# Optimization experiments

Measured on AMD Instinct MI355X. Metric: run time of the kernel, lower is better.

The kernel has to match this reference:

```python
import jax, jax.numpy as jnp
import numpy as np

N, E, G = 10000, 100000, 16
NS, NV = 128, 64            # scalar (0e) / vector (1o) channel counts
DIM = NS + 3 * NV           # 320 flattened feature dim
NSP = 4                     # num_species; edge one-hot has NSP**2 entries
FC_IN = 128                 # edge length embedding size
GATES = NV                  # one gate scalar per gated vector channel
EPS = 1e-5


def _split(x):
    # flattened irreps layout: [NS scalars | NV vectors * 3 components]
    return x[:, :NS], x[:, NS:].reshape(x.shape[0], NV, 3)


def _merge(s, v):
    return jnp.concatenate([s, v.reshape(v.shape[0], -1)], axis=-1)


def setup_inputs() -> dict:
    key = jax.random.key(0)
    ks = jax.random.split(key, 32)
    def nrm(i, shape):
        return jax.random.normal(ks[i], shape, jnp.float32)
    return {
        'node_fea': nrm(0, (N, DIM)),
        'edge_one_hot': jax.random.uniform(ks[1], (E, NSP * NSP), jnp.float32),
        'edge_sh': nrm(2, (E, 4)),
        'edge_fea': nrm(3, (E, DIM)),
        'edge_length_embedded': jax.random.uniform(ks[4], (E, FC_IN), jnp.float32),
        'edge_index': jax.random.randint(ks[5], (2, E), 0, N),
        'batch': jnp.sort(jax.random.randint(ks[6], (N,), 0, G)),
        # self-connection FCTP: edge irreps x species-pair scalars -> out irreps
        'Wsc_s': nrm(7, (NS, NSP * NSP, NS)),
        'Wsc_v': nrm(8, (NV, NSP * NSP, NV)),
        # lin_pre (per-l equivariant linear, bias on scalars only)
        'Wpre0': nrm(9, (NS, NS)), 'bpre0': jnp.zeros((NS,), jnp.float32),
        'Wpre1': nrm(10, (NV, NV)),
        # separate-weight tensor product paths (fea_in x spherical harmonics)
        'Wss': nrm(11, (3 * NS, NS + GATES)),   # 0e x 0e -> 0e
        'Wvs': nrm(12, (3 * NV, NS + GATES)),   # 1o . 1o -> 0e
        'Wsv': nrm(13, (3 * NS, NV)),           # 0e x 1o -> 1o
        'Wvv': nrm(14, (3 * NV, NV)),           # 1o x 0e -> 1o
        # radial MLP (fc): edge_length_embedded -> per-channel conv weights
        'Wf1': nrm(15, (FC_IN, 64)) / np.sqrt(FC_IN), 'bf1': jnp.zeros((64,), jnp.float32),
        'Wf2': nrm(16, (64, 64)) / 8.0, 'bf2': jnp.zeros((64,), jnp.float32),
        'Wf3': nrm(17, (64, NS + NV)) / 8.0, 'bf3': jnp.zeros((NS + NV,), jnp.float32),
        # lin_post
        'Wpost0': nrm(18, (NS, NS)), 'bpost0': jnp.zeros((NS,), jnp.float32),
        'Wpost1': nrm(19, (NV, NV)),
        # e3LayerNorm affine params
        'gamma_s': jnp.ones((NS,), jnp.float32), 'beta_s': jnp.zeros((NS,), jnp.float32),
        'gamma_v': jnp.ones((NV,), jnp.float32),
    }


def reference(node_fea, edge_one_hot, edge_sh, edge_fea, edge_length_embedded,
              edge_index, batch, Wsc_s, Wsc_v, Wpre0, bpre0, Wpre1,
              Wss, Wvs, Wsv, Wvv, Wf1, bf1, Wf2, bf2, Wf3, bf3,
              Wpost0, bpost0, Wpost1, gamma_s, beta_s, gamma_v):
    i, j = edge_index[0], edge_index[1]
    batch_edge = batch[i]
    es, ev = _split(edge_fea)

    # --- self connection: FullyConnectedTensorProduct(edge_fea, one_hot) ---
    sc_s = jnp.einsum('ev,es,vsu->eu', es, edge_one_hot, Wsc_s) / np.sqrt(NS * NSP * NSP)
    sc_v = jnp.einsum('evm,es,vsu->eum', ev, edge_one_hot, Wsc_v) / np.sqrt(NV * NSP * NSP)

    # --- lin_pre on edge features ---
    s = es @ Wpre0 / np.sqrt(NS) + bpre0
    v = jnp.einsum('evm,vu->eum', ev, Wpre1) / np.sqrt(NV)

    # --- gather node features and concat along channel axis ---
    nsf, nvf = _split(node_fea)
    s_in = jnp.concatenate([nsf[i], nsf[j], s], axis=-1)   # [E, 3*NS]
    v_in = jnp.concatenate([nvf[i], nvf[j], v], axis=1)    # [E, 3*NV, 3]

    sh0, sh1 = edge_sh[:, :1], edge_sh[:, 1:4]
    # --- separate-weight tensor product (CG: 1o x 1o -> 0e via dot/sqrt(3)) ---
    out_s = (jnp.einsum('ev,vu->eu', s_in * sh0, Wss) / np.sqrt(3 * NS)
             + jnp.einsum('evm,em,vu->eu', v_in, sh1, Wvs) / np.sqrt(3 * 3 * NV)) / np.sqrt(2.0)
    out_v = (jnp.einsum('ev,em,vu->eum', s_in, sh1, Wsv) / np.sqrt(3 * NS)
             + jnp.einsum('evm,e,vu->eum', v_in, sh0[:, 0], Wvv) / np.sqrt(3 * NV)) / np.sqrt(2.0)

    # --- gate nonlinearity: silu on scalars, sigmoid gates on vectors ---
    z_s = jax.nn.silu(out_s[:, :NS])
    z_v = out_v * jax.nn.sigmoid(out_s[:, NS:])[:, :, None]

    # --- radial MLP -> e3ElementWise per-channel scaling ---
    h = jax.nn.silu(edge_length_embedded @ Wf1 + bf1)
    h = jax.nn.silu(h @ Wf2 + bf2)
    w = h @ Wf3 + bf3                                      # [E, NS+NV]
    z_s = z_s * w[:, :NS]
    z_v = z_v * w[:, NS:, None]

    # --- lin_post ---
    z_s = z_s @ Wpost0 / np.sqrt(NS) + bpost0
    z_v = jnp.einsum('evm,vu->eum', z_v, Wpost1) / np.sqrt(NV)

    # --- add self connection ---
    z_s = z_s + sc_s
    z_v = z_v + sc_v

    # --- e3LayerNorm with per-graph statistics over edges ---
    cnt = jax.ops.segment_sum(jnp.ones((E,), z_s.dtype), batch_edge, num_segments=G)
    cnt = jnp.maximum(cnt, 1.0)
    mean_s = jax.ops.segment_sum(z_s.sum(-1), batch_edge, num_segments=G) / (cnt * NS)
    z_s = z_s - mean_s[batch_edge][:, None]
    var_s = jax.ops.segment_sum((z_s ** 2).sum(-1), batch_edge, num_segments=G) / (cnt * NS)
    z_s = z_s * jax.lax.rsqrt(var_s + EPS)[batch_edge][:, None] * gamma_s + beta_s
    var_v = jax.ops.segment_sum((z_v ** 2).sum((-1, -2)), batch_edge, num_segments=G) / (cnt * NV * 3)
    z_v = z_v * jax.lax.rsqrt(var_v + EPS)[batch_edge][:, None, None] * gamma_v[None, :, None]

    # --- skip connection (same irreps in/out -> plain add) ---
    return edge_fea + _merge(z_s, z_v)
```

## Files before the change

### kernel.cpp

```cpp
#include <hip/hip_runtime.h>
#include <math.h>

typedef unsigned int u32;
typedef unsigned short u16;
typedef __attribute__((ext_vector_type(8))) short bf16x8;
typedef __attribute__((ext_vector_type(4))) float f32x4;

#define E_TOT 100000
constexpr int NS = 128, DIM = 320;

constexpr float SC_S_SCALE = 0.022097086912079608f;
constexpr float SC_V_SCALE = 0.03125f;
constexpr float INV_SQRT128 = 0.08838834764831845f;
constexpr float INV_8 = 0.125f;
constexpr float INV_S384 = 0.05103103630798288f;
constexpr float INV_24 = 0.041666666666666664f;
constexpr float INV_S192 = 0.07216878364870323f;
constexpr float RSQRT2 = 0.7071067811865476f;

#define MFMA __builtin_amdgcn_mfma_f32_16x16x32_bf16
#define F4Z (f32x4){0.f, 0.f, 0.f, 0.f}

__device__ __forceinline__ float sigmoidf_(float x) { return 1.0f / (1.0f + __expf(-x)); }
__device__ __forceinline__ float siluf_(float x) { return x * sigmoidf_(x); }
__device__ __forceinline__ float bf2f(u16 h) {
  u32 u = ((u32)h) << 16;
  return __builtin_bit_cast(float, u);
}
__device__ __forceinline__ u16 f2bf(float f) {
  u32 u = __builtin_bit_cast(u32, f);
  return (u16)((u + 0x7fffu + ((u >> 16) & 1u)) >> 16);
}
__device__ __forceinline__ void gl_lds16(const void* g, void* l) {
  __builtin_amdgcn_global_load_lds((const __attribute__((address_space(1))) u32*)g,
                                   (__attribute__((address_space(3))) u32*)l, 16, 0, 0);
}
__device__ __forceinline__ bf16x8 pack8(float4 r0, float4 r1, float s) {
  bf16x8 a;
  a[0] = (short)f2bf(r0.x * s); a[1] = (short)f2bf(r0.y * s);
  a[2] = (short)f2bf(r0.z * s); a[3] = (short)f2bf(r0.w * s);
  a[4] = (short)f2bf(r1.x * s); a[5] = (short)f2bf(r1.y * s);
  a[6] = (short)f2bf(r1.z * s); a[7] = (short)f2bf(r1.w * s);
  return a;
}
__device__ __forceinline__ void stb(char* base, int row, int rowB, int colByte, u16 v) {
  *(u16*)(base + row * rowB + (colByte ^ ((row & 7) << 4))) = v;
}
__device__ __forceinline__ u16 ldbs(const char* base, int row, int rowB, int colByte) {
  return *(const u16*)(base + row * rowB + (colByte ^ ((row & 7) << 4)));
}
__device__ __forceinline__ bf16x8 ldb8(const char* base, int row, int rowB, int colByte) {
  return *(const bf16x8*)(base + row * rowB + (colByte ^ ((row & 7) << 4)));
}
__device__ __forceinline__ void stb16(char* base, int row, int rowB, int colByte, bf16x8 v) {
  *(bf16x8*)(base + row * rowB + (colByte ^ ((row & 7) << 4))) = v;
}

#define OW_W2S   0
#define OW_BTV   262144
#define OW_PRE0  327680
#define OW_PRE1X 344064
#define OW_SS    380928
#define OW_VS    454656
#define OW_SV    491520
#define OW_VVX   516096
#define OW_F1    626688
#define OW_F2    634880
#define OW_F3    638976
#define OW_P0    651264
#define OW_P1X   667648
#define OW_END   704512

__device__ __forceinline__ void frag_uc(int oo, int K, int& up, int& c) {
  int per = (K >> 5) << 9;
  int nt = oo / per, r = oo % per;
  int kc = r >> 9, r2 = r & 511;
  int ln = r2 >> 3, j = r2 & 7;
  up = nt * 16 + (ln & 15);
  c = kc * 32 + (ln >> 4) * 8 + j;
}

__global__ __launch_bounds__(256) void k_prep(
    const float* __restrict__ Wsc_s, const float* __restrict__ Wsc_v,
    const float* __restrict__ Wpre0, const float* __restrict__ Wpre1,
    const float* __restrict__ Wss, const float* __restrict__ Wvs,
    const float* __restrict__ Wsv, const float* __restrict__ Wvv,
    const float* __restrict__ Wf1, const float* __restrict__ Wf2,
    const float* __restrict__ Wf3, const float* __restrict__ Wpost0,
    const float* __restrict__ Wpost1, u16* __restrict__ dst) {
  int o = blockIdx.x * 256 + threadIdx.x;
  if (o >= OW_END) return;
  float v;
  int up, c;
  if (o < OW_BTV) {
    int u = o >> 11, k = o & 2047, s = k >> 7, vv = k & 127;
    v = Wsc_s[((size_t)(vv * 16 + s)) * 128 + u] * SC_S_SCALE;
  } else if (o < OW_PRE0) {
    int oo = o - OW_BTV; int u = oo >> 10, k = oo & 1023, s = k >> 6, vv = k & 63;
    v = Wsc_v[((size_t)(vv * 16 + s)) * 64 + u] * SC_V_SCALE;
  } else if (o < OW_PRE1X) {
    frag_uc(o - OW_PRE0, 128, up, c);
    v = Wpre0[c * 128 + up] * INV_SQRT128;
  } else if (o < OW_SS) {
    frag_uc(o - OW_PRE1X, 192, up, c);
    int u = up / 3, m = up % 3, vv = c / 3, mp = c % 3;
    v = (m == mp) ? Wpre1[vv * 64 + u] * INV_8 : 0.f;
  } else if (o < OW_VS) {
    frag_uc(o - OW_SS, 384, up, c);
    v = Wss[c * 192 + up] * (INV_S384 * RSQRT2);
  } else if (o < OW_SV) {
    frag_uc(o - OW_VS, 192, up, c);
    v = Wvs[c * 192 + up] * (INV_24 * RSQRT2);
  } else if (o < OW_VVX) {
    frag_uc(o - OW_SV, 384, up, c);
    v = Wsv[c * 64 + up] * (INV_S384 * RSQRT2);
  } else if (o < OW_F1) {
    frag_uc(o - OW_VVX, 576, up, c);
    int u = up / 3, m = up % 3, p = c / 192, r = c % 192, vv = r / 3, mp = r % 3;
    v = (m == mp) ? Wvv[(p * 64 + vv) * 64 + u] * (INV_S192 * RSQRT2) : 0.f;
  } else if (o < OW_F2) {
    frag_uc(o - OW_F1, 128, up, c);
    v = Wf1[c * 64 + up];
  } else if (o < OW_F3) {
    frag_uc(o - OW_F2, 64, up, c);
    v = Wf2[c * 64 + up];
  } else if (o < OW_P0) {
    frag_uc(o - OW_F3, 64, up, c);
    v = Wf3[c * 192 + up];
  } else if (o < OW_P1X) {
    frag_uc(o - OW_P0, 128, up, c);
    v = Wpost0[c * 128 + up] * INV_SQRT128;
  } else {
    frag_uc(o - OW_P1X, 192, up, c);
    int u = up / 3, m = up % 3, vv = c / 3, mp = c % 3;
    v = (m == mp) ? Wpost1[vv * 64 + u] * INV_8 : 0.f;
  }
  dst[o] = f2bf(v);
}

#define MEs 64
__global__ __launch_bounds__(256, 2) void k_sc(
    const float* __restrict__ edge_fea, const float* __restrict__ ohp,
    const u16* __restrict__ W2s, const u16* __restrict__ Btv,
    float* __restrict__ out) {
  __shared__ char esB[16384];
  __shared__ char evT[24576];
  __shared__ float ohL[64][16];
  __shared__ char Bbuf[32768];
  const int t = threadIdx.x, lane = t & 63, ww = t >> 6;
  const int l15 = lane & 15, q8 = lane >> 4, q4 = q8 << 2, cbl = q8 << 4;
  const int e0 = blockIdx.x * MEs;
  const int nE = min(MEs, E_TOT - e0);

  for (int o = t; o < 2560; o += 256) {
    int c = o % 40, e = o / 40;
    float4 r0 = make_float4(0.f, 0.f, 0.f, 0.f), r1 = r0;
    if (e < nE) {
      const float* src = edge_fea + (size_t)(e0 + e) * 320 + c * 8;
      r0 = *(const float4*)src; r1 = *(const float4*)(src + 4);
    }
    if (c < 16) stb16(esB, e, 256, c * 16, pack8(r0, r1, 1.f));
    else {
      int base = (c - 16) * 8;
      float vals[8] = {r0.x, r0.y, r0.z, r0.w, r1.x, r1.y, r1.z, r1.w};
      #pragma unroll
      for (int z = 0; z < 8; ++z) {
        int cc = base + z;
        stb(evT, 3 * e + cc % 3, 128, (cc / 3) * 2, f2bf(vals[z]));
      }
    }
  }
  for (int o = t; o < 1024; o += 256) {
    int e = o >> 4, s = o & 15;
    ohL[e][s] = (e < nE) ? ohp[(size_t)(e0 + e) * 16 + s] : 0.f;
  }
  __syncthreads();

  {
    bf16x8 afh[4][4];
    #pragma unroll
    for (int rt = 0; rt < 4; ++rt)
      #pragma unroll
      for (int ks = 0; ks < 4; ++ks)
        afh[rt][ks] = ldb8(esB, rt * 16 + l15, 256, ks * 64 + cbl);
    f32x4 acc[8];
    #pragma unroll
    for (int i = 0; i < 8; ++i) acc[i] = F4Z;
    for (int s = 0; s < 16; ++s) {
      const char* sb = (const char*)W2s + s * 256;
      #pragma unroll
      for (int it = 0; it < 8; ++it) {
        int n = it * 256 + t;
        int u = n >> 4, gp = n & 15, g = gp ^ (u & 7);
        gl_lds16(sb + (size_t)u * 4096 + g * 16, Bbuf + n * 16);
      }
      __syncthreads();
      f32x4 tmp[8];
      #pragma unroll
      for (int i = 0; i < 8; ++i) tmp[i] = F4Z;
      #pragma unroll
      for (int ks = 0; ks < 4; ++ks) {
        bf16x8 b0 = ldb8(Bbuf, ww * 32 + l15, 256, ks * 64 + cbl);
        bf16x8 b1 = ldb8(Bbuf, ww * 32 + 16 + l15, 256, ks * 64 + cbl);
        #pragma unroll
        for (int rt = 0; rt < 4; ++rt) {
          tmp[rt * 2 + 0] = MFMA(afh[rt][ks], b0, tmp[rt * 2 + 0], 0, 0, 0);
          tmp[rt * 2 + 1] = MFMA(afh[rt][ks], b1, tmp[rt * 2 + 1], 0, 0, 0);
        }
      }
      #pragma unroll
      for (int rt = 0; rt < 4; ++rt)
        #pragma unroll
        for (int j = 0; j < 4; ++j) {
          float oh = ohL[rt * 16 + q4 + j][s];
          acc[rt * 2 + 0][j] += oh * tmp[rt * 2 + 0][j];
          acc[rt * 2 + 1][j] += oh * tmp[rt * 2 + 1][j];
        }
      __syncthreads();
    }
    #pragma unroll
    for (int rt = 0; rt < 4; ++rt)
      #pragma unroll
      for (int ct = 0; ct < 2; ++ct) {
        int u = ww * 32 + ct * 16 + l15;
        #pragma unroll
        for (int j = 0; j < 4; ++j) {
          int e = rt * 16 + q4 + j;
          if (e < nE) out[(size_t)(e0 + e) * DIM + u] = acc[rt * 2 + ct][j];
        }
      }
  }

  {
    f32x4 acc[12];
    #pragma unroll
    for (int i = 0; i < 12; ++i) acc[i] = F4Z;
    for (int s = 0; s < 16; ++s) {
      #pragma unroll
      for (int it = 0; it < 2; ++it) {
        int n = it * 256 + t;
        int u = n >> 3, gp = n & 7, g = gp ^ (u & 7);
        gl_lds16((const char*)Btv + (size_t)u * 2048 + s * 128 + g * 16, Bbuf + n * 16);
      }
      __syncthreads();
      f32x4 tmp[12];
      #pragma unroll
      for (int i = 0; i < 12; ++i) tmp[i] = F4Z;
      #pragma unroll
      for (int ks = 0; ks < 2; ++ks) {
        bf16x8 b = ldb8(Bbuf, ww * 16 + l15, 128, ks * 64 + cbl);
        #pragma unroll
        for (int rt = 0; rt < 12; ++rt) {
          bf16x8 a = ldb8(evT, rt * 16 + l15, 128, ks * 64 + cbl);
          tmp[rt] = MFMA(a, b, tmp[rt], 0, 0, 0);
        }
      }
      #pragma unroll
      for (int rt = 0; rt < 12; ++rt)
        #pragma unroll
        for (int j = 0; j < 4; ++j) {
          int r = rt * 16 + q4 + j;
          acc[rt][j] += ohL[r / 3][s] * tmp[rt][j];
        }
      __syncthreads();
    }
    int u = ww * 16 + l15;
    #pragma unroll
    for (int rt = 0; rt < 12; ++rt)
      #pragma unroll
      for (int j = 0; j < 4; ++j) {
        int r = rt * 16 + q4 + j, e = r / 3, m = r - e * 3;
        if (e < nE) out[(size_t)(e0 + e) * DIM + 128 + u * 3 + m] = acc[rt][j];
      }
  }
}

#define A_SZ 78976
__global__ __launch_bounds__(512, 4) void k_chain(
    const float* __restrict__ node_fea, const float* __restrict__ edge_sh,
    const float* __restrict__ edge_fea, const float* __restrict__ elen,
    const int* __restrict__ eidx, const int* __restrict__ batch,
    const u16* __restrict__ wbf,
    const float* __restrict__ bpre0, const float* __restrict__ bf1,
    const float* __restrict__ bf2, const float* __restrict__ bf3,
    const float* __restrict__ bpost0, float* __restrict__ out,
    float* __restrict__ statsB) {
  __shared__ char AR[A_SZ];
  float* shF = (float*)(AR + 77824);
  int* ijL = (int*)(AR + 78336);
  float* sS  = (float*)(AR + 78592);
  float* sS2 = (float*)(AR + 78720);
  float* sV  = (float*)(AR + 78848);
  const int t = threadIdx.x, lane = t & 63, wv = t >> 6;
  const int l15 = lane & 15, q8 = lane >> 4, q4 = q8 << 2, cbl = q8 << 4;
  const int e0 = blockIdx.x * 32;

#define SA(b) (AR + (b) * 8192)
#define VA(b) (AR + 24576 + (b) * 12288)
  char* wB = AR;
  char* zsB = AR + 12288;
  char* gateB = AR + 20480;
  char* zvB = AR + 24576;
  char* t1B = AR + 61440;
  char* hB = AR + 65536;
  char* elB = AR + 69632;

  if (t < 64) { int p = t >> 5, e = t & 31; ijL[p * 32 + e] = eidx[p * E_TOT + e0 + e]; }
  if (t >= 64 && t < 192) { int o = t - 64; shF[o] = edge_sh[(size_t)e0 * 4 + o]; }
  if (t >= 192 && t < 288) ((float*)(AR + 78592))[t - 192] = 0.f;
  __syncthreads();

  for (int o = t; o < 1280; o += 512) {
    int c = o % 40, e = o / 40;
    const float* src = edge_fea + (size_t)(e0 + e) * 320 + c * 8;
    float4 r0 = *(const float4*)src, r1 = *(const float4*)(src + 4);
    bf16x8 v = pack8(r0, r1, 1.f);
    if (c < 16) stb16(SA(2), e, 256, c * 16, v);
    else        stb16(VA(2), e, 384, (c - 16) * 16, v);
  }
  for (int o = t; o < 2560; o += 512) {
    int c = o % 40, tmp = o / 40, e = tmp & 31, p = tmp >> 5;
    const float* src = node_fea + (size_t)ijL[p * 32 + e] * 320 + c * 8;
    float4 r0 = *(const float4*)src, r1 = *(const float4*)(src + 4);
    bf16x8 v = pack8(r0, r1, 1.f);
    if (c < 16) stb16(SA(p), e, 256, c * 16, v);
    else        stb16(VA(p), e, 384, (c - 16) * 16, v);
  }
  for (int o = t; o < 512; o += 512) {
    int c = o & 15, e = o >> 4;
    const float* src = elen + (size_t)(e0 + e) * 128 + c * 8;
    float4 r0 = *(const float4*)src, r1 = *(const float4*)(src + 4);
    stb16(elB, e, 256, c * 16, pack8(r0, r1, 1.f));
  }
  __syncthreads();

  f32x4 acc[8];
  #pragma unroll
  for (int a = 0; a < 8; ++a) acc[a] = F4Z;
  if (wv < 4) {
    for (int kc = 0; kc < 6; ++kc) {
      bf16x8 a0 = ldb8(VA(2), l15, 384, kc * 64 + cbl);
      bf16x8 a1 = ldb8(VA(2), 16 + l15, 384, kc * 64 + cbl);
      #pragma unroll
      for (int i = 0; i < 3; ++i) {
        int nt = wv * 3 + i;
        bf16x8 b = *(const bf16x8*)(wbf + OW_PRE1X + (((size_t)nt * 6 + kc) << 9) + lane * 8);
        acc[i] = MFMA(a0, b, acc[i], 0, 0, 0);
        acc[3 + i] = MFMA(a1, b, acc[3 + i], 0, 0, 0);
      }
    }
  } else if (wv < 6) {
    for (int kc = 0; kc < 4; ++kc) {
      bf16x8 a0 = ldb8(SA(2), l15, 256, kc * 64 + cbl);
      bf16x8 a1 = ldb8(SA(2), 16 + l15, 256, kc * 64 + cbl);
      #pragma unroll
      for (int i = 0; i < 4; ++i) {
        int nt = (wv - 4) * 4 + i;
        bf16x8 b = *(const bf16x8*)(wbf + OW_PRE0 + (((size_t)nt * 4 + kc) << 9) + lane * 8);
        acc[i] = MFMA(a0, b, acc[i], 0, 0, 0);
        acc[4 + i] = MFMA(a1, b, acc[4 + i], 0, 0, 0);
      }
    }
  } else {
    for (int kc = 0; kc < 4; ++kc) {
      bf16x8 a0 = ldb8(elB, l15, 256, kc * 64 + cbl);
      bf16x8 a1 = ldb8(elB, 16 + l15, 256, kc * 64 + cbl);
      #pragma unroll
      for (int i = 0; i < 2; ++i) {
        int nt = (wv - 6) * 2 + i;
        bf16x8 b = *(const bf16x8*)(wbf + OW_F1 + (((size_t)nt * 4 + kc) << 9) + lane * 8);
        acc[i] = MFMA(a0, b, acc[i], 0, 0, 0);
        acc[2 + i] = MFMA(a1, b, acc[2 + i], 0, 0, 0);
      }
    }
  }
  __syncthreads();
  if (wv < 4) {
    #pragma unroll
    for (int mt = 0; mt < 2; ++mt)
      #pragma unroll
      for (int i = 0; i < 3; ++i) {
        int up = (wv * 3 + i) * 16 + l15;
        #pragma unroll
        for (int j = 0; j < 4; ++j)
          stb(VA(2), mt * 16 + q4 + j, 384, up * 2, f2bf(acc[mt * 3 + i][j]));
      }
  } else if (wv < 6) {
    #pragma unroll
    for (int i = 0; i < 4; ++i) {
      int u = ((wv - 4) * 4 + i) * 16 + l15;
      float bias = bpre0[u];
      #pragma unroll
      for (int mt = 0; mt < 2; ++mt)
        #pragma unroll
        for (int j = 0; j < 4; ++j)
          stb(SA(2), mt * 16 + q4 + j, 256, u * 2, f2bf(acc[mt * 4 + i][j] + bias));
    }
  } else {
    #pragma unroll
    for (int i = 0; i < 2; ++i) {
      int u = ((wv - 6) * 2 + i) * 16 + l15;
      float bias = bf1[u];
      #pragma unroll
      for (int mt = 0; mt < 2; ++mt)
        #pragma unroll
        for (int j = 0; j < 4; ++j)
          stb(hB, mt * 16 + q4 + j, 128, u * 2, f2bf(siluf_(acc[mt * 2 + i][j] + bias)));
    }
  }
  __syncthreads();

  for (int o = t; o < 32 * 192; o += 512) {
    int e = o / 192, K = o % 192;
    int src = K >> 6, kk = K & 63;
    const char* vb = VA(src);
    float x0 = bf2f(ldbs(vb, e, 384, (3 * kk + 0) * 2));
    float x1 = bf2f(ldbs(vb, e, 384, (3 * kk + 1) * 2));
    float x2 = bf2f(ldbs(vb, e, 384, (3 * kk + 2) * 2));
    float sv = x0 * shF[e * 4 + 1] + x1 * shF[e * 4 + 2] + x2 * shF[e * 4 + 3];
    if (K < 128) stb(elB, e, 256, K * 2, f2bf(sv));
    else stb(t1B, e, 128, (K - 128) * 2, f2bf(sv));
  }
  __syncthreads();

  f32x4 os[4] = {F4Z, F4Z, F4Z, F4Z};
  f32x4 h2a = F4Z;
  {
    const int hmt = wv >> 2, hnt = wv & 3;
    #pragma unroll
    for (int kc = 0; kc < 2; ++kc) {
      bf16x8 a = ldb8(hB, hmt * 16 + l15, 128, kc * 64 + cbl);
      bf16x8 b = *(const bf16x8*)(wbf + OW_F2 + (((size_t)hnt * 2 + kc) << 9) + lane * 8);
      h2a = MFMA(a, b, h2a, 0, 0, 0);
    }
  }
  if (wv < 6) {
    for (int kc = 0; kc < 12; ++kc) {
      int buf = kc >> 2, cB = (kc & 3) * 64 + cbl;
      bf16x8 a0 = ldb8(SA(buf), l15, 256, cB);
      bf16x8 a1 = ldb8(SA(buf), 16 + l15, 256, cB);
      #pragma unroll
      for (int i = 0; i < 2; ++i) {
        int nt = wv * 2 + i;
        bf16x8 b = *(const bf16x8*)(wbf + OW_SS + (((size_t)nt * 12 + kc) << 9) + lane * 8);
        os[i] = MFMA(a0, b, os[i], 0, 0, 0);
        os[2 + i] = MFMA(a1, b, os[2 + i], 0, 0, 0);
      }
    }
    #pragma unroll
    for (int mt = 0; mt < 2; ++mt)
      #pragma unroll
      for (int i = 0; i < 2; ++i)
        #pragma unroll
        for (int j = 0; j < 4; ++j)
          os[mt * 2 + i][j] *= shF[(mt * 16 + q4 + j) * 4 + 0];
    for (int kc = 0; kc < 6; ++kc) {
      const char* sb_ = (kc < 4) ? elB : t1B;
      int rB = (kc < 4) ? 256 : 128;
      int cB = ((kc < 4) ? kc : (kc - 4)) * 64 + cbl;
      bf16x8 a0 = ldb8(sb_, l15, rB, cB);
      bf16x8 a1 = ldb8(sb_, 16 + l15, rB, cB);
      #pragma unroll
      for (int i = 0; i < 2; ++i) {
        int nt = wv * 2 + i;
        bf16x8 b = *(const bf16x8*)(wbf + OW_VS + (((size_t)nt * 6 + kc) << 9) + lane * 8);
        os[i] = MFMA(a0, b, os[i], 0, 0, 0);
        os[2 + i] = MFMA(a1, b, os[2 + i], 0, 0, 0);
      }
    }
  } else {
    for (int kc = 0; kc < 12; ++kc) {
      int buf = kc >> 2, cB = (kc & 3) * 64 + cbl;
      bf16x8 a0 = ldb8(SA(buf), l15, 256, cB);
      bf16x8 a1 = ldb8(SA(buf), 16 + l15, 256, cB);
      #pragma unroll
      for (int i = 0; i < 2; ++i) {
        int nt = (wv - 6) * 2 + i;
        bf16x8 b = *(const bf16x8*)(wbf + OW_SV + (((size_t)nt * 12 + kc) << 9) + lane * 8);
        os[i] = MFMA(a0, b, os[i], 0, 0, 0);
        os[2 + i] = MFMA(a1, b, os[2 + i], 0, 0, 0);
      }
    }
  }
  __syncthreads();
  {
    const int hmt = wv >> 2;
    int u = (wv & 3) * 16 + l15;
    float bias = bf2[u];
    #pragma unroll
    for (int j = 0; j < 4; ++j)
      stb(hB, hmt * 16 + q4 + j, 128, u * 2, f2bf(siluf_(h2a[j] + bias)));
  }
  if (wv >= 6) {
    #pragma unroll
    for (int mt = 0; mt < 2; ++mt)
      #pragma unroll
      for (int i = 0; i < 2; ++i) {
        int u = ((wv - 6) * 2 + i) * 16 + l15;
        #pragma unroll
        for (int j = 0; j < 4; ++j)
          stb(t1B, mt * 16 + q4 + j, 128, u * 2, f2bf(os[mt * 2 + i][j]));
      }
  }
  __syncthreads();

  {
    f32x4 wa[3] = {F4Z, F4Z, F4Z};
    const int mtw = wv >> 2;
    #pragma unroll
    for (int kc = 0; kc < 2; ++kc) {
      bf16x8 a = ldb8(hB, mtw * 16 + l15, 128, kc * 64 + cbl);
      #pragma unroll
      for (int i = 0; i < 3; ++i) {
        int nt = (wv & 3) * 3 + i;
        bf16x8 b = *(const bf16x8*)(wbf + OW_F3 + (((size_t)nt * 2 + kc) << 9) + lane * 8);
        wa[i] = MFMA(a, b, wa[i], 0, 0, 0);
      }
    }
    #pragma unroll
    for (int i = 0; i < 3; ++i) {
      int up = ((wv & 3) * 3 + i) * 16 + l15;
      float bias = bf3[up];
      #pragma unroll
      for (int j = 0; j < 4; ++j)
        stb(wB, mtw * 16 + q4 + j, 384, up * 2, f2bf(wa[i][j] + bias));
    }
  }
  __syncthreads();

  if (wv < 6) {
    #pragma unroll
    for (int mt = 0; mt < 2; ++mt)
      #pragma unroll
      for (int i = 0; i < 2; ++i) {
        int up = (wv * 2 + i) * 16 + l15;
        #pragma unroll
        for (int j = 0; j < 4; ++j) {
          int e = mt * 16 + q4 + j;
          float w_ = bf2f(ldbs(wB, e, 384, up * 2));
          float o_ = os[mt * 2 + i][j];
          if (up < 128) stb(zsB, e, 256, up * 2, f2bf(siluf_(o_) * w_));
          else stb(gateB, e, 128, (up - 128) * 2, f2bf(sigmoidf_(o_) * w_));
        }
      }
  }
  f32x4 ov[3] = {F4Z, F4Z, F4Z};
  {
    const int mtv = wv >> 2;
    for (int p = 0; p < 3; ++p)
      for (int kc6 = 0; kc6 < 6; ++kc6) {
        int cB = kc6 * 64 + cbl;
        bf16x8 a = ldb8(VA(p), mtv * 16 + l15, 384, cB);
        int kcg = p * 6 + kc6;
        #pragma unroll
        for (int i = 0; i < 3; ++i) {
          int nt = (wv & 3) * 3 + i;
          bf16x8 b = *(const bf16x8*)(wbf + OW_VVX + (((size_t)nt * 18 + kcg) << 9) + lane * 8);
          ov[i] = MFMA(a, b, ov[i], 0, 0, 0);
        }
      }
  }
  __syncthreads();
  {
    const int mtv = wv >> 2;
    #pragma unroll
    for (int i = 0; i < 3; ++i) {
      int up = ((wv & 3) * 3 + i) * 16 + l15;
      int u = (up * 683) >> 11, m = up - 3 * u;
      #pragma unroll
      for (int j = 0; j < 4; ++j) {
        int e = mtv * 16 + q4 + j;
        float t1v = bf2f(ldbs(t1B, e, 128, u * 2));
        float g = bf2f(ldbs(gateB, e, 128, u * 2));
        float val = ov[i][j] * shF[e * 4 + 0] + t1v * shF[e * 4 + 1 + m];
        stb(zvB, e, 384, up * 2, f2bf(val * g));
      }
    }
  }
  __syncthreads();

  {
    f32x4 p0[2] = {F4Z, F4Z};
    #pragma unroll
    for (int kc = 0; kc < 4; ++kc) {
      int cB = kc * 64 + cbl;
      bf16x8 a0 = ldb8(zsB, l15, 256, cB);
      bf16x8 a1 = ldb8(zsB, 16 + l15, 256, cB);
      bf16x8 b = *(const bf16x8*)(wbf + OW_P0 + (((size_t)wv * 4 + kc) << 9) + lane * 8);
      p0[0] = MFMA(a0, b, p0[0], 0, 0, 0);
      p0[1] = MFMA(a1, b, p0[1], 0, 0, 0);
    }
    int u = wv * 16 + l15;
    float bias = bpost0[u];
    float s1p[8], s2p[8];
    #pragma unroll
    for (int mt = 0; mt < 2; ++mt)
      #pragma unroll
      for (int j = 0; j < 4; ++j) {
        size_t o = (size_t)(e0 + mt * 16 + q4 + j) * DIM + u;
        float z = out[o] + p0[mt][j] + bias;
        out[o] = z;
        s1p[mt * 4 + j] = z;
        s2p[mt * 4 + j] = z * z;
      }
    #pragma unroll
    for (int msk = 1; msk < 16; msk <<= 1)
      #pragma unroll
      for (int k = 0; k < 8; ++k) {
        s1p[k] += __shfl_xor(s1p[k], msk);
        s2p[k] += __shfl_xor(s2p[k], msk);
      }
    if (l15 == 0) {
      #pragma unroll
      for (int mt = 0; mt < 2; ++mt)
        #pragma unroll
        for (int j = 0; j < 4; ++j) {
          int e = mt * 16 + q4 + j;
          atomicAdd(&sS[e], s1p[mt * 4 + j]);
          atomicAdd(&sS2[e], s2p[mt * 4 + j]);
        }
    }
  }
  {
    f32x4 p1[3] = {F4Z, F4Z, F4Z};
    const int mtv = wv >> 2;
    #pragma unroll
    for (int kc = 0; kc < 6; ++kc) {
      int cB = kc * 64 + cbl;
      bf16x8 a = ldb8(zvB, mtv * 16 + l15, 384, cB);
      #pragma unroll
      for (int i = 0; i < 3; ++i) {
        int nt = (wv & 3) * 3 + i;
        bf16x8 b = *(const bf16x8*)(wbf + OW_P1X + (((size_t)nt * 6 + kc) << 9) + lane * 8);
        p1[i] = MFMA(a, b, p1[i], 0, 0, 0);
      }
    }
    float svp[4] = {0.f, 0.f, 0.f, 0.f};
    #pragma unroll
    for (int i = 0; i < 3; ++i) {
      int up = ((wv & 3) * 3 + i) * 16 + l15;
      #pragma unroll
      for (int j = 0; j < 4; ++j) {
        size_t o = (size_t)(e0 + mtv * 16 + q4 + j) * DIM + 128 + up;
        float z = out[o] + p1[i][j];
        out[o] = z;
        svp[j] += z * z;
      }
    }
    #pragma unroll
    for (int msk = 1; msk < 16; msk <<= 1)
      #pragma unroll
      for (int j = 0; j < 4; ++j) svp[j] += __shfl_xor(svp[j], msk);
    if (l15 == 0) {
      #pragma unroll
      for (int j = 0; j < 4; ++j)
        atomicAdd(&sV[mtv * 16 + q4 + j], svp[j]);
    }
  }
  __syncthreads();
  if (t < 32) {
    int g = batch[ijL[t]];
    float* sb = statsB + ((size_t)(blockIdx.x & 63)) * 64 + g * 4;
    atomicAdd(sb + 0, 1.0f);
    atomicAdd(sb + 1, sS[t]);
    atomicAdd(sb + 2, sS2[t]);
    atomicAdd(sb + 3, sV[t]);
  }
#undef SA
#undef VA
}

__global__ __launch_bounds__(256) void k_norm(
    const float* __restrict__ edge_fea, const int* __restrict__ eidx,
    const int* __restrict__ batch, const float* __restrict__ stats,
    const float* __restrict__ gamma_s, const float* __restrict__ beta_s,
    const float* __restrict__ gamma_v, float* __restrict__ out) {
  __shared__ float meanL[16], invsL[16], invvL[16];
  __shared__ int gL[16];
  const int t = threadIdx.x;
  const int e0 = blockIdx.x * 16;
  if (t < 16) {
    float c = 0.f, a = 0.f, b = 0.f, d = 0.f;
    for (int q = 0; q < 64; ++q) {
      const float* p = stats + (size_t)q * 64 + t * 4;
      c += p[0]; a += p[1]; b += p[2]; d += p[3];
    }
    float cnt = fmaxf(c, 1.0f);
    float m = a / (cnt * 128.0f);
    float var = b / (cnt * 128.0f) - m * m;
    meanL[t] = m;
    invsL[t] = rsqrtf(var + 1e-5f);
    invvL[t] = rsqrtf(d / (cnt * 192.0f) + 1e-5f);
  }
  if (t >= 32 && t < 48) gL[t - 32] = batch[eidx[e0 + t - 32]];
  __syncthreads();
  for (int o = t; o < 16 * 80; o += 256) {
    int e = o / 80, q = o % 80;
    size_t idx = (size_t)(e0 + e) * 80 + q;
    float4 z = ((const float4*)out)[idx];
    float4 ef = ((const float4*)edge_fea)[idx];
    int g = gL[e];
    float4 r;
    if (q < 32) {
      int c = q * 4;
      r.x = (z.x - meanL[g]) * invsL[g] * gamma_s[c + 0] + beta_s[c + 0] + ef.x;
      r.y = (z.y - meanL[g]) * invsL[g] * gamma_s[c + 1] + beta_s[c + 1] + ef.y;
      r.z = (z.z - meanL[g]) * invsL[g] * gamma_s[c + 2] + beta_s[c + 2] + ef.z;
      r.w = (z.w - meanL[g]) * invsL[g] * gamma_s[c + 3] + beta_s[c + 3] + ef.w;
    } else {
      int cc = q * 4 - 128;
      r.x = z.x * invvL[g] * gamma_v[(cc + 0) / 3] + ef.x;
      r.y = z.y * invvL[g] * gamma_v[(cc + 1) / 3] + ef.y;
      r.z = z.z * invvL[g] * gamma_v[(cc + 2) / 3] + ef.z;
      r.w = z.w * invvL[g] * gamma_v[(cc + 3) / 3] + ef.w;
    }
    ((float4*)out)[idx] = r;
  }
}

extern "C" void kernel_launch(void* const* d_in, const int* in_sizes, int n_in,
                              void* d_out, int out_size, void* d_ws, size_t ws_size,
                              hipStream_t stream) {
  const float* node_fea = (const float*)d_in[0];
  const float* edge_oh  = (const float*)d_in[1];
  const float* edge_sh  = (const float*)d_in[2];
  const float* edge_fea = (const float*)d_in[3];
  const float* elen     = (const float*)d_in[4];
  const int*   eidx     = (const int*)d_in[5];
  const int*   batch    = (const int*)d_in[6];
  const float* Wsc_s    = (const float*)d_in[7];
  const float* Wsc_v    = (const float*)d_in[8];
  const float* Wpre0    = (const float*)d_in[9];
  const float* bpre0    = (const float*)d_in[10];
  const float* Wpre1    = (const float*)d_in[11];
  const float* Wss      = (const float*)d_in[12];
  const float* Wvs      = (const float*)d_in[13];
  const float* Wsv      = (const float*)d_in[14];
  const float* Wvv      = (const float*)d_in[15];
  const float* Wf1      = (const float*)d_in[16];
  const float* bf1      = (const float*)d_in[17];
  const float* Wf2      = (const float*)d_in[18];
  const float* bf2      = (const float*)d_in[19];
  const float* Wf3      = (const float*)d_in[20];
  const float* bf3      = (const float*)d_in[21];
  const float* Wpost0   = (const float*)d_in[22];
  const float* bpost0   = (const float*)d_in[23];
  const float* Wpost1   = (const float*)d_in[24];
  const float* gamma_s  = (const float*)d_in[25];
  const float* beta_s   = (const float*)d_in[26];
  const float* gamma_v  = (const float*)d_in[27];
  float* out = (float*)d_out;

  char* ws = (char*)d_ws;
  float* statsB = (float*)ws;
  u16* wbf = (u16*)(ws + 16384);

  hipMemsetAsync(statsB, 0, 64 * 64 * sizeof(float), stream);
  k_prep<<<(OW_END + 255) / 256, 256, 0, stream>>>(
      Wsc_s, Wsc_v, Wpre0, Wpre1, Wss, Wvs, Wsv, Wvv,
      Wf1, Wf2, Wf3, Wpost0, Wpost1, wbf);
  const int nblk64 = (E_TOT + MEs - 1) / MEs;
  k_sc<<<nblk64, 256, 0, stream>>>(edge_fea, edge_oh, wbf + OW_W2S, wbf + OW_BTV, out);
  k_chain<<<E_TOT / 32, 512, 0, stream>>>(node_fea, edge_sh, edge_fea, elen, eidx, batch,
                                          wbf, bpre0, bf1, bf2, bf3, bpost0, out, statsB);
  k_norm<<<E_TOT / 16, 256, 0, stream>>>(edge_fea, eidx, batch, statsB,
                                         gamma_s, beta_s, gamma_v, out);
}
```

Measured before the change: 652.7 us.

## Prepack self-connection weights into MFMA fragment order and load directly from global

The prep kernel now writes the self-connection weights in per-lane MFMA B-fragment order, so the k_sc kernel loads each B fragment straight from global memory with one 16-byte load. This removes the shared-memory staging buffer and the two barriers per species iteration. The block grows to 512 threads, with each wave owning 16 output columns and the vector path split into row halves. The aim is less LDS traffic, fewer syncs and higher occupancy, at the cost of repeated global or L2 weight reads per block and A fragments reloaded from LDS on every iteration.

New measurement: 2.269 ms. +247.6%, slower.

```diff
diff --git a/kernel.cpp b/kernel.cpp
--- a/kernel.cpp
+++ b/kernel.cpp
@@ -93,10 +93,17 @@
   float v;
   int up, c;
   if (o < OW_BTV) {
-    int u = o >> 11, k = o & 2047, s = k >> 7, vv = k & 127;
+    int idx = o >> 9, j = o & 7, ln = (o >> 3) & 63;
+    int kc = idx & 3, nt = (idx >> 2) & 7, s = idx >> 5;
+    int u = nt * 16 + (ln & 15);
+    int vv = kc * 32 + (ln >> 4) * 8 + j;
     v = Wsc_s[((size_t)(vv * 16 + s)) * 128 + u] * SC_S_SCALE;
   } else if (o < OW_PRE0) {
-    int oo = o - OW_BTV; int u = oo >> 10, k = oo & 1023, s = k >> 6, vv = k & 63;
+    int oo = o - OW_BTV;
+    int idx = oo >> 9, j = oo & 7, ln = (oo >> 3) & 63;
+    int kc = idx & 1, nt = (idx >> 1) & 3, s = idx >> 3;
+    int u = nt * 16 + (ln & 15);
+    int vv = kc * 32 + (ln >> 4) * 8 + j;
     v = Wsc_v[((size_t)(vv * 16 + s)) * 64 + u] * SC_V_SCALE;
   } else if (o < OW_PRE1X) {
     frag_uc(o - OW_PRE0, 128, up, c);
@@ -139,20 +146,19 @@
 }
 
 #define MEs 64
-__global__ __launch_bounds__(256, 2) void k_sc(
+__global__ __launch_bounds__(512, 6) void k_sc(
     const float* __restrict__ edge_fea, const float* __restrict__ ohp,
-    const u16* __restrict__ W2s, const u16* __restrict__ Btv,
+    const u16* __restrict__ Wfs, const u16* __restrict__ Wfv,
     float* __restrict__ out) {
   __shared__ char esB[16384];
   __shared__ char evT[24576];
   __shared__ float ohL[64][16];
-  __shared__ char Bbuf[32768];
   const int t = threadIdx.x, lane = t & 63, ww = t >> 6;
   const int l15 = lane & 15, q8 = lane >> 4, q4 = q8 << 2, cbl = q8 << 4;
   const int e0 = blockIdx.x * MEs;
   const int nE = min(MEs, E_TOT - e0);
 
-  for (int o = t; o < 2560; o += 256) {
+  for (int o = t; o < 2560; o += 512) {
     int c = o % 40, e = o / 40;
     float4 r0 = make_float4(0.f, 0.f, 0.f, 0.f), r1 = r0;
     if (e < nE) {
@@ -170,107 +176,75 @@
       }
     }
   }
-  for (int o = t; o < 1024; o += 256) {
+  for (int o = t; o < 1024; o += 512) {
     int e = o >> 4, s = o & 15;
     ohL[e][s] = (e < nE) ? ohp[(size_t)(e0 + e) * 16 + s] : 0.f;
   }
   __syncthreads();
 
   {
-    bf16x8 afh[4][4];
+    f32x4 acc[4] = {F4Z, F4Z, F4Z, F4Z};
+    for (int s = 0; s < 16; ++s) {
+      bf16x8 B[4];
+      #pragma unroll
+      for (int kc = 0; kc < 4; ++kc)
+        B[kc] = *(const bf16x8*)(Wfs + ((((size_t)s * 8 + ww) * 4 + kc) << 9) + lane * 8);
+      f32x4 tmp[4] = {F4Z, F4Z, F4Z, F4Z};
+      #pragma unroll
+      for (int kc = 0; kc < 4; ++kc)
+        #pragma unroll
+        for (int rt = 0; rt < 4; ++rt) {
+          bf16x8 a = ldb8(esB, rt * 16 + l15, 256, kc * 64 + cbl);
+          tmp[rt] = MFMA(a, B[kc], tmp[rt], 0, 0, 0);
+        }
+      #pragma unroll
+      for (int rt = 0; rt < 4; ++rt)
+        #pragma unroll
+        for (int j = 0; j < 4; ++j)
+          acc[rt][j] += ohL[rt * 16 + q4 + j][s] * tmp[rt][j];
+    }
+    int u = ww * 16 + l15;
     #pragma unroll
     for (int rt = 0; rt < 4; ++rt)
       #pragma unroll
-      for (int ks = 0; ks < 4; ++ks)
-        afh[rt][ks] = ldb8(esB, rt * 16 + l15, 256, ks * 64 + cbl);
-    f32x4 acc[8];
-    #pragma unroll
-    for (int i = 0; i < 8; ++i) acc[i] = F4Z;
+      for (int j = 0; j < 4; ++j) {
+        int e = rt * 16 + q4 + j;
+        if (e < nE) out[(size_t)(e0 + e) * DIM + u] = acc[rt][j];
+      }
+  }
+
+  {
+    const int colt = ww & 3, rb = (ww >> 2) * 6;
+    f32x4 acc[6] = {F4Z, F4Z, F4Z, F4Z, F4Z, F4Z};
     for (int s = 0; s < 16; ++s) {
-      const char* sb = (const char*)W2s + s * 256;
-      #pragma unroll
-      for (int it = 0; it < 8; ++it) {
-        int n = it * 256 + t;
-        int u = n >> 4, gp = n & 15, g = gp ^ (u & 7);
-        gl_lds16(sb + (size_t)u * 4096 + g * 16, Bbuf + n * 16);
-      }
-      __syncthreads();
-      f32x4 tmp[8];
-      #pragma unroll
-      for (int i = 0; i < 8; ++i) tmp[i] = F4Z;
-      #pragma unroll
-      for (int ks = 0; ks < 4; ++ks) {
-        bf16x8 b0 = ldb8(Bbuf, ww * 32 + l15, 256, ks * 64 + cbl);
-        bf16x8 b1 = ldb8(Bbuf, ww * 32 + 16 + l15, 256, ks * 64 + cbl);
-        #pragma unroll
-        for (int rt = 0; rt < 4; ++rt) {
-          tmp[rt * 2 + 0] = MFMA(afh[rt][ks], b0, tmp[rt * 2 + 0], 0, 0, 0);
-          tmp[rt * 2 + 1] = MFMA(afh[rt][ks], b1, tmp[rt * 2 + 1], 0, 0, 0);
+      bf16x8 B[2];
+      #pragma unroll
+      for (int kc = 0; kc < 2; ++kc)
+        B[kc] = *(const bf16x8*)(Wfv + ((((size_t)s * 4 + colt) * 2 + kc) << 9) + lane * 8);
+      f32x4 tmp[6] = {F4Z, F4Z, F4Z, F4Z, F4Z, F4Z};
+      #pragma unroll
+      for (int kc = 0; kc < 2; ++kc)
+        #pragma unroll
+        for (int i = 0; i < 6; ++i) {
+          bf16x8 a = ldb8(evT, (rb + i) * 16 + l15, 128, kc * 64 + cbl);
+          tmp[i] = MFMA(a, B[kc], tmp[i], 0, 0, 0);
         }
-      }
-      #pragma unroll
-      for (int rt = 0; rt < 4; ++rt)
+      #pragma unroll
+      for (int i = 0; i < 6; ++i)
         #pragma unroll
         for (int j = 0; j < 4; ++j) {
-          float oh = ohL[rt * 16 + q4 + j][s];
-          acc[rt * 2 + 0][j] += oh * tmp[rt * 2 + 0][j];
-          acc[rt * 2 + 1][j] += oh * tmp[rt * 2 + 1][j];
+          int r = (rb + i) * 16 + q4 + j;
+          acc[i][j] += ohL[(r * 683) >> 11][s] * tmp[i][j];
         }
-      __syncthreads();
-    }
-    #pragma unroll
-    for (int rt = 0; rt < 4; ++rt)
-      #pragma unroll
-      for (int ct = 0; ct < 2; ++ct) {
-        int u = ww * 32 + ct * 16 + l15;
-        #pragma unroll
-        for (int j = 0; j < 4; ++j) {
-          int e = rt * 16 + q4 + j;
-          if (e < nE) out[(size_t)(e0 + e) * DIM + u] = acc[rt * 2 + ct][j];
-        }
-      }
-  }
-
-  {
-    f32x4 acc[12];
-    #pragma unroll
-    for (int i = 0; i < 12; ++i) acc[i] = F4Z;
-    for (int s = 0; s < 16; ++s) {
-      #pragma unroll
-      for (int it = 0; it < 2; ++it) {
-        int n = it * 256 + t;
-        int u = n >> 3, gp = n & 7, g = gp ^ (u & 7);
-        gl_lds16((const char*)Btv + (size_t)u * 2048 + s * 128 + g * 16, Bbuf + n * 16);
-      }
-      __syncthreads();
-      f32x4 tmp[12];
-      #pragma unroll
-      for (int i = 0; i < 12; ++i) tmp[i] = F4Z;
-      #pragma unroll
-      for (int ks = 0; ks < 2; ++ks) {
-        bf16x8 b = ldb8(Bbuf, ww * 16 + l15, 128, ks * 64 + cbl);
-        #pragma unroll
-        for (int rt = 0; rt < 12; ++rt) {
-          bf16x8 a = ldb8(evT, rt * 16 + l15, 128, ks * 64 + cbl);
-          tmp[rt] = MFMA(a, b, tmp[rt], 0, 0, 0);
-        }
-      }
-      #pragma unroll
-      for (int rt = 0; rt < 12; ++rt)
-        #pragma unroll
-        for (int j = 0; j < 4; ++j) {
-          int r = rt * 16 + q4 + j;
-          acc[rt][j] += ohL[r / 3][s] * tmp[rt][j];
-        }
-      __syncthreads();
-    }
-    int u = ww * 16 + l15;
-    #pragma unroll
-    for (int rt = 0; rt < 12; ++rt)
+    }
+    int u = colt * 16 + l15;
+    #pragma unroll
+    for (int i = 0; i < 6; ++i)
       #pragma unroll
       for (int j = 0; j < 4; ++j) {
-        int r = rt * 16 + q4 + j, e = r / 3, m = r - e * 3;
-        if (e < nE) out[(size_t)(e0 + e) * DIM + 128 + u * 3 + m] = acc[rt][j];
+        int r = (rb + i) * 16 + q4 + j;
+        int e = (r * 683) >> 11, m = r - 3 * e;
+        if (e < nE) out[(size_t)(e0 + e) * DIM + 128 + u * 3 + m] = acc[i][j];
       }
   }
 }
@@ -760,7 +734,7 @@
       Wsc_s, Wsc_v, Wpre0, Wpre1, Wss, Wvs, Wsv, Wvv,
       Wf1, Wf2, Wf3, Wpost0, Wpost1, wbf);
   const int nblk64 = (E_TOT + MEs - 1) / MEs;
-  k_sc<<<nblk64, 256, 0, stream>>>(edge_fea, edge_oh, wbf + OW_W2S, wbf + OW_BTV, out);
+  k_sc<<<nblk64, 512, 0, stream>>>(edge_fea, edge_oh, wbf + OW_W2S, wbf + OW_BTV, out);
   k_chain<<<E_TOT / 32, 512, 0, stream>>>(node_fea, edge_sh, edge_fea, elen, eidx, batch,
                                           wbf, bpre0, bf1, bf2, bf3, bpost0, out, statsB);
   k_norm<<<E_TOT / 16, 256, 0, stream>>>(edge_fea, eidx, batch, statsB,
```

## Split self-connection kernel into scalar and vector kernels with retuned tiling

Applied to the files above, without the earlier changes.

The fused self-connection kernel is split in two. The scalar part now processes 128 edges per block, which halves how often the per-species 32KB weight tile is reloaded per edge. The vector part runs as its own kernel with a smaller LDS footprint and launch bounds raised to 4 blocks per CU for higher occupancy. The trade-off is an extra kernel launch, edge_fea and one-hot being read twice, and the scalar A fragments now reloaded from LDS instead of held in registers.

After: 855.3 us. 31.0% more time.

```diff
diff --git a/kernel.cpp b/kernel.cpp
--- a/kernel.cpp
+++ b/kernel.cpp
@@ -138,36 +138,106 @@
   dst[o] = f2bf(v);
 }
 
+__global__ __launch_bounds__(256, 2) void k_sc_s(
+    const float* __restrict__ edge_fea, const float* __restrict__ ohp,
+    const u16* __restrict__ W2s, float* __restrict__ out) {
+  __shared__ char esB[32768];
+  __shared__ float ohL[128][16];
+  __shared__ char Bbuf[32768];
+  const int t = threadIdx.x, lane = t & 63, ww = t >> 6;
+  const int l15 = lane & 15, q8 = lane >> 4, q4 = q8 << 2, cbl = q8 << 4;
+  const int e0 = blockIdx.x * 128;
+  const int nE = min(128, E_TOT - e0);
+
+  for (int o = t; o < 2048; o += 256) {
+    int c = o & 15, e = o >> 4;
+    float4 r0 = make_float4(0.f, 0.f, 0.f, 0.f), r1 = r0;
+    if (e < nE) {
+      const float* src = edge_fea + (size_t)(e0 + e) * 320 + c * 8;
+      r0 = *(const float4*)src; r1 = *(const float4*)(src + 4);
+    }
+    stb16(esB, e, 256, c * 16, pack8(r0, r1, 1.f));
+  }
+  for (int o = t; o < 2048; o += 256) {
+    int e = o >> 4, s = o & 15;
+    ohL[e][s] = (e < nE) ? ohp[(size_t)(e0 + e) * 16 + s] : 0.f;
+  }
+  __syncthreads();
+
+  f32x4 acc[8][2];
+  #pragma unroll
+  for (int rt = 0; rt < 8; ++rt) { acc[rt][0] = F4Z; acc[rt][1] = F4Z; }
+  for (int s = 0; s < 16; ++s) {
+    const char* sb = (const char*)W2s + s * 256;
+    #pragma unroll
+    for (int it = 0; it < 8; ++it) {
+      int n = it * 256 + t;
+      int u = n >> 4, gp = n & 15, g = gp ^ (u & 7);
+      gl_lds16(sb + (size_t)u * 4096 + g * 16, Bbuf + n * 16);
+    }
+    __syncthreads();
+    f32x4 tmp[8][2];
+    #pragma unroll
+    for (int rt = 0; rt < 8; ++rt) { tmp[rt][0] = F4Z; tmp[rt][1] = F4Z; }
+    #pragma unroll
+    for (int ks = 0; ks < 4; ++ks) {
+      bf16x8 b0 = ldb8(Bbuf, ww * 32 + l15, 256, ks * 64 + cbl);
+      bf16x8 b1 = ldb8(Bbuf, ww * 32 + 16 + l15, 256, ks * 64 + cbl);
+      #pragma unroll
+      for (int rt = 0; rt < 8; ++rt) {
+        bf16x8 a = ldb8(esB, rt * 16 + l15, 256, ks * 64 + cbl);
+        tmp[rt][0] = MFMA(a, b0, tmp[rt][0], 0, 0, 0);
+        tmp[rt][1] = MFMA(a, b1, tmp[rt][1], 0, 0, 0);
+      }
+    }
+    #pragma unroll
+    for (int rt = 0; rt < 8; ++rt)
+      #pragma unroll
+      for (int j = 0; j < 4; ++j) {
+        float oh = ohL[rt * 16 + q4 + j][s];
+        acc[rt][0][j] += oh * tmp[rt][0][j];
+        acc[rt][1][j] += oh * tmp[rt][1][j];
+      }
+    __syncthreads();
+  }
+  #pragma unroll
+  for (int rt = 0; rt < 8; ++rt)
+    #pragma unroll
+    for (int ct = 0; ct < 2; ++ct) {
+      int u = ww * 32 + ct * 16 + l15;
+      #pragma unroll
+      for (int j = 0; j < 4; ++j) {
+        int e = rt * 16 + q4 + j;
+        if (e < nE) out[(size_t)(e0 + e) * DIM + u] = acc[rt][ct][j];
+      }
+    }
+}
+
 #define MEs 64
-__global__ __launch_bounds__(256, 2) void k_sc(
+__global__ __launch_bounds__(256, 4) void k_sc_v(
     const float* __restrict__ edge_fea, const float* __restrict__ ohp,
-    const u16* __restrict__ W2s, const u16* __restrict__ Btv,
-    float* __restrict__ out) {
-  __shared__ char esB[16384];
+    const u16* __restrict__ Btv, float* __restrict__ out) {
   __shared__ char evT[24576];
   __shared__ float ohL[64][16];
-  __shared__ char Bbuf[32768];
+  __shared__ char Bbuf[8192];
   const int t = threadIdx.x, lane = t & 63, ww = t >> 6;
   const int l15 = lane & 15, q8 = lane >> 4, q4 = q8 << 2, cbl = q8 << 4;
   const int e0 = blockIdx.x * MEs;
   const int nE = min(MEs, E_TOT - e0);
 
-  for (int o = t; o < 2560; o += 256) {
-    int c = o % 40, e = o / 40;
+  for (int o = t; o < 64 * 24; o += 256) {
+    int c = o % 24, e = o / 24;
     float4 r0 = make_float4(0.f, 0.f, 0.f, 0.f), r1 = r0;
     if (e < nE) {
-      const float* src = edge_fea + (size_t)(e0 + e) * 320 + c * 8;
+      const float* src = edge_fea + (size_t)(e0 + e) * 320 + 128 + c * 8;
       r0 = *(const float4*)src; r1 = *(const float4*)(src + 4);
     }
-    if (c < 16) stb16(esB, e, 256, c * 16, pack8(r0, r1, 1.f));
-    else {
-      int base = (c - 16) * 8;
-      float vals[8] = {r0.x, r0.y, r0.z, r0.w, r1.x, r1.y, r1.z, r1.w};
-      #pragma unroll
-      for (int z = 0; z < 8; ++z) {
-        int cc = base + z;
-        stb(evT, 3 * e + cc % 3, 128, (cc / 3) * 2, f2bf(vals[z]));
-      }
+    int base = c * 8;
+    float vals[8] = {r0.x, r0.y, r0.z, r0.w, r1.x, r1.y, r1.z, r1.w};
+    #pragma unroll
+    for (int z = 0; z < 8; ++z) {
+      int cc = base + z;
+      stb(evT, 3 * e + cc % 3, 128, (cc / 3) * 2, f2bf(vals[z]));
     }
   }
   for (int o = t; o < 1024; o += 256) {
@@ -176,103 +246,46 @@
   }
   __syncthreads();
 
-  {
-    bf16x8 afh[4][4];
-    #pragma unroll
-    for (int rt = 0; rt < 4; ++rt)
-      #pragma unroll
-      for (int ks = 0; ks < 4; ++ks)
-        afh[rt][ks] = ldb8(esB, rt * 16 + l15, 256, ks * 64 + cbl);
-    f32x4 acc[8];
-    #pragma unroll
-    for (int i = 0; i < 8; ++i) acc[i] = F4Z;
-    for (int s = 0; s < 16; ++s) {
-      const char* sb = (const char*)W2s + s * 256;
-      #pragma unroll
-      for (int it = 0; it < 8; ++it) {
-        int n = it * 256 + t;
-        int u = n >> 4, gp = n & 15, g = gp ^ (u & 7);
-        gl_lds16(sb + (size_t)u * 4096 + g * 16, Bbuf + n * 16);
-      }
-      __syncthreads();
-      f32x4 tmp[8];
-      #pragma unroll
-      for (int i = 0; i < 8; ++i) tmp[i] = F4Z;
-      #pragma unroll
-      for (int ks = 0; ks < 4; ++ks) {
-        bf16x8 b0 = ldb8(Bbuf, ww * 32 + l15, 256, ks * 64 + cbl);
-        bf16x8 b1 = ldb8(Bbuf, ww * 32 + 16 + l15, 256, ks * 64 + cbl);
-        #pragma unroll
-        for (int rt = 0; rt < 4; ++rt) {
-          tmp[rt * 2 + 0] = MFMA(afh[rt][ks], b0, tmp[rt * 2 + 0], 0, 0, 0);
-          tmp[rt * 2 + 1] = MFMA(afh[rt][ks], b1, tmp[rt * 2 + 1], 0, 0, 0);
-        }
-      }
-      #pragma unroll
-      for (int rt = 0; rt < 4; ++rt)
-        #pragma unroll
-        for (int j = 0; j < 4; ++j) {
-          float oh = ohL[rt * 16 + q4 + j][s];
-          acc[rt * 2 + 0][j] += oh * tmp[rt * 2 + 0][j];
-          acc[rt * 2 + 1][j] += oh * tmp[rt * 2 + 1][j];
-        }
-      __syncthreads();
-    }
-    #pragma unroll
-    for (int rt = 0; rt < 4; ++rt)
-      #pragma unroll
-      for (int ct = 0; ct < 2; ++ct) {
-        int u = ww * 32 + ct * 16 + l15;
-        #pragma unroll
-        for (int j = 0; j < 4; ++j) {
-          int e = rt * 16 + q4 + j;
-          if (e < nE) out[(size_t)(e0 + e) * DIM + u] = acc[rt * 2 + ct][j];
-        }
-      }
-  }
-
-  {
-    f32x4 acc[12];
-    #pragma unroll
-    for (int i = 0; i < 12; ++i) acc[i] = F4Z;
-    for (int s = 0; s < 16; ++s) {
-      #pragma unroll
-      for (int it = 0; it < 2; ++it) {
-        int n = it * 256 + t;
-        int u = n >> 3, gp = n & 7, g = gp ^ (u & 7);
-        gl_lds16((const char*)Btv + (size_t)u * 2048 + s * 128 + g * 16, Bbuf + n * 16);
-      }
-      __syncthreads();
-      f32x4 tmp[12];
-      #pragma unroll
-      for (int i = 0; i < 12; ++i) tmp[i] = F4Z;
-      #pragma unroll
-      for (int ks = 0; ks < 2; ++ks) {
-        bf16x8 b = ldb8(Bbuf, ww * 16 + l15, 128, ks * 64 + cbl);
-        #pragma unroll
-        for (int rt = 0; rt < 12; ++rt) {
-          bf16x8 a = ldb8(evT, rt * 16 + l15, 128, ks * 64 + cbl);
-          tmp[rt] = MFMA(a, b, tmp[rt], 0, 0, 0);
-        }
-      }
-      #pragma unroll
-      for (int rt = 0; rt < 12; ++rt)
-        #pragma unroll
-        for (int j = 0; j < 4; ++j) {
-          int r = rt * 16 + q4 + j;
-          acc[rt][j] += ohL[r / 3][s] * tmp[rt][j];
-        }
-      __syncthreads();
-    }
-    int u = ww * 16 + l15;
+  f32x4 acc[12];
+  #pragma unroll
+  for (int i = 0; i < 12; ++i) acc[i] = F4Z;
+  for (int s = 0; s < 16; ++s) {
+    #pragma unroll
+    for (int it = 0; it < 2; ++it) {
+      int n = it * 256 + t;
+      int u = n >> 3, gp = n & 7, g = gp ^ (u & 7);
+      gl_lds16((const char*)Btv + (size_t)u * 2048 + s * 128 + g * 16, Bbuf + n * 16);
+    }
+    __syncthreads();
+    f32x4 tmp[12];
+    #pragma unroll
+    for (int i = 0; i < 12; ++i) tmp[i] = F4Z;
+    #pragma unroll
+    for (int ks = 0; ks < 2; ++ks) {
+      bf16x8 b = ldb8(Bbuf, ww * 16 + l15, 128, ks * 64 + cbl);
+      #pragma unroll
+      for (int rt = 0; rt < 12; ++rt) {
+        bf16x8 a = ldb8(evT, rt * 16 + l15, 128, ks * 64 + cbl);
+        tmp[rt] = MFMA(a, b, tmp[rt], 0, 0, 0);
+      }
+    }
     #pragma unroll
     for (int rt = 0; rt < 12; ++rt)
       #pragma unroll
       for (int j = 0; j < 4; ++j) {
-        int r = rt * 16 + q4 + j, e = r / 3, m = r - e * 3;
-        if (e < nE) out[(size_t)(e0 + e) * DIM + 128 + u * 3 + m] = acc[rt][j];
-      }
-  }
+        int r = rt * 16 + q4 + j;
+        acc[rt][j] += ohL[r / 3][s] * tmp[rt][j];
+      }
+    __syncthreads();
+  }
+  int u = ww * 16 + l15;
+  #pragma unroll
+  for (int rt = 0; rt < 12; ++rt)
+    #pragma unroll
+    for (int j = 0; j < 4; ++j) {
+      int r = rt * 16 + q4 + j, e = r / 3, m = r - e * 3;
+      if (e < nE) out[(size_t)(e0 + e) * DIM + 128 + u * 3 + m] = acc[rt][j];
+    }
 }
 
 #define A_SZ 78976
@@ -759,8 +772,8 @@
   k_prep<<<(OW_END + 255) / 256, 256, 0, stream>>>(
       Wsc_s, Wsc_v, Wpre0, Wpre1, Wss, Wvs, Wsv, Wvv,
       Wf1, Wf2, Wf3, Wpost0, Wpost1, wbf);
-  const int nblk64 = (E_TOT + MEs - 1) / MEs;
-  k_sc<<<nblk64, 256, 0, stream>>>(edge_fea, edge_oh, wbf + OW_W2S, wbf + OW_BTV, out);
+  k_sc_s<<<(E_TOT + 127) / 128, 256, 0, stream>>>(edge_fea, edge_oh, wbf + OW_W2S, out);
+  k_sc_v<<<(E_TOT + MEs - 1) / MEs, 256, 0, stream>>>(edge_fea, edge_oh, wbf + OW_BTV, out);
   k_chain<<<E_TOT / 32, 512, 0, stream>>>(node_fea, edge_sh, edge_fea, elen, eidx, batch,
                                           wbf, bpre0, bf1, bf2, bf3, bpost0, out, statsB);
   k_norm<<<E_TOT / 16, 256, 0, stream>>>(edge_fea, eidx, batch, statsB,
```
